# Optimization experiments

Hardware: AMD Instinct MI355X
Metric: run time of the kernel (lower is better)

Reference implementation:

```python
import jax, jax.numpy as jnp
import numpy as np

N_NODES = 50000
F_IN = 256
HEADS = 8
C = 256 // HEADS  # out channels per head (output_dim // heads)
NEG_SLOPE = 0.2


def setup_inputs() -> dict:
    key = jax.random.key(0)
    k_x, k_e, k_w, k_as, k_ad, k_b = jax.random.split(key, 6)
    x = jax.random.normal(k_x, (N_NODES, F_IN), dtype=jnp.float32)
    edge_index = jax.random.randint(k_e, (2, 800000), 0, N_NODES, dtype=jnp.int32)
    # GATConv params: linear weight, per-head attention vectors, bias
    s = 1.0 / np.sqrt(F_IN)
    W = jax.random.uniform(k_w, (F_IN, HEADS * C), jnp.float32, -s, s)
    att_src = jax.random.uniform(k_as, (HEADS, C), jnp.float32, -s, s)
    att_dst = jax.random.uniform(k_ad, (HEADS, C), jnp.float32, -s, s)
    bias = jnp.zeros((HEADS * C,), jnp.float32)
    return {"x": x, "edge_index": edge_index, "W": W,
            "att_src": att_src, "att_dst": att_dst, "bias": bias}


def _gat_forward(x, edge_index, W, att_src, att_dst, bias):
    N = x.shape[0]
    # add self loops (PyG GATConv default add_self_loops=True)
    loops = jnp.arange(N, dtype=edge_index.dtype)
    src = jnp.concatenate([edge_index[0], loops])
    dst = jnp.concatenate([edge_index[1], loops])

    h = (x @ W).reshape(N, HEADS, C)                       # [N,H,C]
    a_src = jnp.einsum('nhc,hc->nh', h, att_src)           # [N,H]
    a_dst = jnp.einsum('nhc,hc->nh', h, att_dst)           # [N,H]

    alpha = a_src[src] + a_dst[dst]                        # [E2,H]
    alpha = jax.nn.leaky_relu(alpha, NEG_SLOPE)
    # softmax over incoming edges of each dst node, per head
    amax = jax.ops.segment_max(alpha, dst, num_segments=N)
    amax = jnp.where(jnp.isfinite(amax), amax, 0.0)
    ex = jnp.exp(alpha - amax[dst])
    denom = jax.ops.segment_sum(ex, dst, num_segments=N) + 1e-16
    attn = ex / denom[dst]                                 # [E2,H]

    msg = h[src] * attn[:, :, None]                        # [E2,H,C]
    out = jax.ops.segment_sum(msg, dst, num_segments=N)    # [N,H,C]
    out = out.reshape(N, HEADS * C) + bias
    return jax.nn.elu(out)


def reference(x, edge_index, W, att_src, att_dst, bias):
    return _gat_forward(x, edge_index, W, att_src, att_dst, bias)
```

## Files before the change

kernel.cpp:

```cpp
#include <hip/hip_runtime.h>
#include <hip/hip_bf16.h>
#include <math.h>

#define F_IN 256
#define HEADS 8
#define CPH 32
#define NEG_SLOPE 0.2f
#define MAXD 128

typedef short bf16x8 __attribute__((ext_vector_type(8)));
typedef float f32x4  __attribute__((ext_vector_type(4)));
typedef _Float16 half4 __attribute__((ext_vector_type(4)));

static __device__ __forceinline__ unsigned short f2bf(float f) {
    union { float f; unsigned int u; } v; v.f = f;
    unsigned int r = (v.u + 0x7FFFu + ((v.u >> 16) & 1u)) >> 16;
    return (unsigned short)r;
}
static __device__ __forceinline__ float bf2f(unsigned short h) {
    union { unsigned int u; float f; } v; v.u = ((unsigned int)h) << 16;
    return v.f;
}

static __device__ __forceinline__ void lds_fence() {
    asm volatile("s_waitcnt lgkmcnt(0)" ::: "memory");
    __builtin_amdgcn_sched_barrier(0);
}

__global__ __launch_bounds__(256) void wprep_kernel(
    const float* __restrict__ W, short* __restrict__ WtHi, short* __restrict__ WtLo)
{
    const int k = blockIdx.x;
    const int n = threadIdx.x;
    const float w = W[(size_t)k * 256 + n];
    const unsigned short h = f2bf(w);
    const unsigned short l = f2bf(w - bf2f(h));
    const int step = k >> 5, kg = (k >> 3) & 3, j = k & 7;
    const size_t dst = ((((size_t)step * 4 + kg) * 256) + n) * 8 + j;
    WtHi[dst] = (short)h;
    WtLo[dst] = (short)l;
}

__global__ __launch_bounds__(256, 2) void gemm_mfma_kernel(
    const float* __restrict__ X, const short* __restrict__ WtHi,
    const short* __restrict__ WtLo, _Float16* __restrict__ H2, int M)
{
    __shared__ short Ah[4][128][8];
    __shared__ short Al[4][128][8];
    __shared__ short Bh[4][128][8];
    __shared__ short Bl[4][128][8];

    const int t    = threadIdx.x;
    const int lane = t & 63;
    const int wid  = t >> 6;
    const int wr   = wid >> 1;
    const int wc   = wid & 1;
    const int row0 = blockIdx.x * 128;
    const int col0 = blockIdx.y * 128;

    const int srow  = t >> 1;
    const int shalf = t & 1;

    f32x4 acc[4][4];
#pragma unroll
    for (int i = 0; i < 4; ++i)
#pragma unroll
        for (int j = 0; j < 4; ++j)
            acc[i][j] = (f32x4){0.f, 0.f, 0.f, 0.f};

    const int kgf = lane >> 4;
    const int lrow = lane & 15;

    for (int step = 0; step < 8; ++step) {
        const int k0 = step * 32;
        float f[16];
        const int grow = row0 + srow;
        if (grow < M) {
            const float4* xp = (const float4*)(X + (size_t)grow * 256 + k0 + shalf * 16);
            const float4 v0 = xp[0], v1 = xp[1], v2 = xp[2], v3 = xp[3];
            f[0] = v0.x; f[1] = v0.y; f[2]  = v0.z; f[3]  = v0.w;
            f[4] = v1.x; f[5] = v1.y; f[6]  = v1.z; f[7]  = v1.w;
            f[8] = v2.x; f[9] = v2.y; f[10] = v2.z; f[11] = v2.w;
            f[12] = v3.x; f[13] = v3.y; f[14] = v3.z; f[15] = v3.w;
        } else {
#pragma unroll
            for (int j = 0; j < 16; ++j) f[j] = 0.f;
        }
#pragma unroll
        for (int c = 0; c < 2; ++c) {
            bf16x8 hi, lo;
#pragma unroll
            for (int j = 0; j < 8; ++j) {
                const float x = f[c * 8 + j];
                const unsigned short hb = f2bf(x);
                hi[j] = (short)hb;
                lo[j] = (short)f2bf(x - bf2f(hb));
            }
            const int kg = shalf * 2 + c;
            *(bf16x8*)&Ah[kg][srow][0] = hi;
            *(bf16x8*)&Al[kg][srow][0] = lo;
        }
#pragma unroll
        for (int rep = 0; rep < 2; ++rep) {
            const int s  = t + rep * 256;
            const int kg = s >> 7;
            const int nl = s & 127;
            const size_t src = ((((size_t)step * 4 + kg) * 256) + col0 + nl) * 8;
            *(bf16x8*)&Bh[kg][nl][0] = *(const bf16x8*)&WtHi[src];
            *(bf16x8*)&Bl[kg][nl][0] = *(const bf16x8*)&WtLo[src];
        }
        __syncthreads();

        bf16x8 ah[4], al[4];
#pragma unroll
        for (int i = 0; i < 4; ++i) {
            const int rl = wr * 64 + i * 16 + lrow;
            ah[i] = *(const bf16x8*)&Ah[kgf][rl][0];
            al[i] = *(const bf16x8*)&Al[kgf][rl][0];
        }
#pragma unroll
        for (int j = 0; j < 4; ++j) {
            const int cl = wc * 64 + j * 16 + lrow;
            const bf16x8 bh = *(const bf16x8*)&Bh[kgf][cl][0];
            const bf16x8 bl = *(const bf16x8*)&Bl[kgf][cl][0];
#pragma unroll
            for (int i = 0; i < 4; ++i) {
                acc[i][j] = __builtin_amdgcn_mfma_f32_16x16x32_bf16(al[i], bh, acc[i][j], 0, 0, 0);
                acc[i][j] = __builtin_amdgcn_mfma_f32_16x16x32_bf16(ah[i], bl, acc[i][j], 0, 0, 0);
                acc[i][j] = __builtin_amdgcn_mfma_f32_16x16x32_bf16(ah[i], bh, acc[i][j], 0, 0, 0);
            }
        }
        __syncthreads();
    }

    const int cbase = col0 + wc * 64 + lrow;
    const int rbase = row0 + wr * 64 + (lane >> 4) * 4;
#pragma unroll
    for (int i = 0; i < 4; ++i) {
#pragma unroll
        for (int r = 0; r < 4; ++r) {
            const int row = rbase + i * 16 + r;
            if (row < M) {
#pragma unroll
                for (int j = 0; j < 4; ++j)
                    H2[(size_t)row * 256 + cbase + j * 16] = (_Float16)acc[i][j][r];
            }
        }
    }
}

__global__ __launch_bounds__(256) void attdot_kernel(
    const _Float16* __restrict__ H2, const float* __restrict__ att_src,
    const float* __restrict__ att_dst, float* __restrict__ a_src,
    float* __restrict__ a_dst, int N)
{
    const int n = (int)((blockIdx.x * blockDim.x + threadIdx.x) >> 6);
    const int lane = threadIdx.x & 63;
    if (n >= N) return;
    const half4 hv = *(const half4*)(H2 + (size_t)n * 256 + lane * 4);
    const float4 as = *(const float4*)(att_src + lane * 4);
    const float4 ad = *(const float4*)(att_dst + lane * 4);
    const float h0 = (float)hv[0], h1 = (float)hv[1], h2 = (float)hv[2], h3 = (float)hv[3];
    float s = h0 * as.x + h1 * as.y + h2 * as.z + h3 * as.w;
    float d = h0 * ad.x + h1 * ad.y + h2 * ad.z + h3 * ad.w;
#pragma unroll
    for (int off = 1; off < 8; off <<= 1) {
        s += __shfl_xor(s, off);
        d += __shfl_xor(d, off);
    }
    if ((lane & 7) == 0) {
        a_src[(size_t)n * 8 + (lane >> 3)] = s;
        a_dst[(size_t)n * 8 + (lane >> 3)] = d;
    }
}

__global__ __launch_bounds__(256) void hist_kernel(
    const int* __restrict__ ei, int* __restrict__ deg, int E, int E2)
{
    const int e = blockIdx.x * blockDim.x + threadIdx.x;
    if (e >= E2) return;
    const int dst = (e < E) ? ei[(size_t)E + e] : (e - E);
    atomicAdd(&deg[dst], 1);
}

__global__ __launch_bounds__(256) void scan_reduce_kernel(
    const int* __restrict__ deg, int* __restrict__ partial, int n)
{
    const int i = blockIdx.x * 256 + threadIdx.x;
    int v = (i < n) ? deg[i] : 0;
#pragma unroll
    for (int off = 1; off < 64; off <<= 1) v += __shfl_xor(v, off);
    __shared__ int s[4];
    if ((threadIdx.x & 63) == 0) s[threadIdx.x >> 6] = v;
    __syncthreads();
    if (threadIdx.x == 0) partial[blockIdx.x] = s[0] + s[1] + s[2] + s[3];
}

__global__ __launch_bounds__(256) void scan_partials_kernel(
    int* __restrict__ partial, int nb)
{
    __shared__ int tmp[256];
    const int t = threadIdx.x;
    const int v = (t < nb) ? partial[t] : 0;
    tmp[t] = v;
    __syncthreads();
    for (int off = 1; off < 256; off <<= 1) {
        int add = (t >= off) ? tmp[t - off] : 0;
        __syncthreads();
        tmp[t] += add;
        __syncthreads();
    }
    if (t < nb) partial[t] = tmp[t] - v;
}

__global__ __launch_bounds__(256) void scan_final_kernel(
    const int* __restrict__ deg, const int* __restrict__ partial,
    int* __restrict__ offsets, int n, int total)
{
    __shared__ int tmp[256];
    const int t = threadIdx.x;
    const int i = blockIdx.x * 256 + t;
    const int v = (i < n) ? deg[i] : 0;
    tmp[t] = v;
    __syncthreads();
    for (int off = 1; off < 256; off <<= 1) {
        int add = (t >= off) ? tmp[t - off] : 0;
        __syncthreads();
        tmp[t] += add;
        __syncthreads();
    }
    if (i < n) offsets[i] = partial[blockIdx.x] + tmp[t] - v;
    if (i == 0) offsets[n] = total;
}

__global__ __launch_bounds__(256) void scatter_kernel(
    const int* __restrict__ ei, const int* __restrict__ offsets,
    int* __restrict__ cursor, int* __restrict__ sorted_src, int E, int E2)
{
    const int e = blockIdx.x * blockDim.x + threadIdx.x;
    if (e >= E2) return;
    int src, dst;
    if (e < E) { src = ei[e]; dst = ei[(size_t)E + e]; }
    else       { src = e - E; dst = e - E; }
    const int pos = atomicAdd(&cursor[dst], 1);
    sorted_src[offsets[dst] + pos] = src;
}

__global__ __launch_bounds__(256) void aggregate_kernel(
    const _Float16* __restrict__ H2, const float* __restrict__ Asrc,
    const float* __restrict__ Adst, const int* __restrict__ offsets,
    const int* __restrict__ sorted_src, const float* __restrict__ bias,
    float* __restrict__ out, int N)
{
    __shared__ float aw[4][MAXD][8];
    __shared__ int   sid[4][MAXD];

    const int n = (int)((blockIdx.x * blockDim.x + threadIdx.x) >> 6);
    const int lane = threadIdx.x & 63;
    const int wid  = (threadIdx.x >> 6) & 3;
    if (n >= N) return;

    const int beg = offsets[n];
    const int deg = offsets[n + 1] - beg;
    const int dcap = deg < MAXD ? deg : MAXD;

    const int h2 = lane & 7;
    const float adst2 = Adst[(size_t)n * 8 + h2];

    float m = -INFINITY;
    for (int i = lane; i < deg * 8; i += 64) {
        const int e = i >> 3;
        const int s = sorted_src[beg + e];
        float a = Asrc[(size_t)s * 8 + h2] + adst2;
        a = a > 0.f ? a : NEG_SLOPE * a;
        if (e < MAXD) {
            aw[wid][e][h2] = a;
            if (h2 == 0) sid[wid][e] = s;
        }
        m = fmaxf(m, a);
    }
#pragma unroll
    for (int off = 8; off < 64; off <<= 1) m = fmaxf(m, __shfl_xor(m, off));
    lds_fence();

    float ssum = 0.f;
    for (int i = lane; i < deg * 8; i += 64) {
        const int e = i >> 3;
        float a;
        if (e < MAXD) {
            a = aw[wid][e][h2];
        } else {
            const int s = sorted_src[beg + e];
            a = Asrc[(size_t)s * 8 + h2] + adst2;
            a = a > 0.f ? a : NEG_SLOPE * a;
        }
        const float w = __expf(a - m);
        ssum += w;
        if (e < MAXD) aw[wid][e][h2] = w;
    }
#pragma unroll
    for (int off = 8; off < 64; off <<= 1) ssum += __shfl_xor(ssum, off);
    const float rdn = 1.f / (ssum + 1e-16f);
    lds_fence();

    for (int i = lane; i < dcap * 8; i += 64)
        aw[wid][i >> 3][h2] *= rdn;
    lds_fence();

    const int h3 = lane >> 3;
    const float m3   = __shfl(m, h3);
    const float rdn3 = __shfl(rdn, h3);
    const float adst3 = __shfl(adst2, h3);

    float4 acc0 = make_float4(0.f, 0.f, 0.f, 0.f);
    float4 acc1 = make_float4(0.f, 0.f, 0.f, 0.f);
    int e = 0;
    for (; e + 4 <= dcap; e += 4) {
        const int4 s4 = *(const int4*)&sid[wid][e];
        const float w0 = aw[wid][e + 0][h3];
        const float w1 = aw[wid][e + 1][h3];
        const float w2 = aw[wid][e + 2][h3];
        const float w3 = aw[wid][e + 3][h3];
        const half4 g0 = *(const half4*)(H2 + (size_t)s4.x * 256 + lane * 4);
        const half4 g1 = *(const half4*)(H2 + (size_t)s4.y * 256 + lane * 4);
        const half4 g2 = *(const half4*)(H2 + (size_t)s4.z * 256 + lane * 4);
        const half4 g3 = *(const half4*)(H2 + (size_t)s4.w * 256 + lane * 4);
        acc0.x += (float)g0[0] * w0; acc0.y += (float)g0[1] * w0; acc0.z += (float)g0[2] * w0; acc0.w += (float)g0[3] * w0;
        acc1.x += (float)g1[0] * w1; acc1.y += (float)g1[1] * w1; acc1.z += (float)g1[2] * w1; acc1.w += (float)g1[3] * w1;
        acc0.x += (float)g2[0] * w2; acc0.y += (float)g2[1] * w2; acc0.z += (float)g2[2] * w2; acc0.w += (float)g2[3] * w2;
        acc1.x += (float)g3[0] * w3; acc1.y += (float)g3[1] * w3; acc1.z += (float)g3[2] * w3; acc1.w += (float)g3[3] * w3;
    }
    for (; e < dcap; ++e) {
        const int s0 = sid[wid][e];
        const float w0 = aw[wid][e][h3];
        const half4 g0 = *(const half4*)(H2 + (size_t)s0 * 256 + lane * 4);
        acc0.x += (float)g0[0] * w0; acc0.y += (float)g0[1] * w0; acc0.z += (float)g0[2] * w0; acc0.w += (float)g0[3] * w0;
    }
    for (; e < deg; ++e) {
        const int s0 = sorted_src[beg + e];
        float a0 = Asrc[(size_t)s0 * 8 + h3] + adst3;
        a0 = a0 > 0.f ? a0 : NEG_SLOPE * a0;
        const float w0 = __expf(a0 - m3) * rdn3;
        const half4 g0 = *(const half4*)(H2 + (size_t)s0 * 256 + lane * 4);
        acc0.x += (float)g0[0] * w0; acc0.y += (float)g0[1] * w0; acc0.z += (float)g0[2] * w0; acc0.w += (float)g0[3] * w0;
    }
    float4 acc;
    acc.x = acc0.x + acc1.x; acc.y = acc0.y + acc1.y;
    acc.z = acc0.z + acc1.z; acc.w = acc0.w + acc1.w;

    const float4 b = *(const float4*)(bias + lane * 4);
    float4 o;
    o.x = acc.x + b.x; o.y = acc.y + b.y; o.z = acc.z + b.z; o.w = acc.w + b.w;
    o.x = o.x > 0.f ? o.x : __expf(o.x) - 1.f;
    o.y = o.y > 0.f ? o.y : __expf(o.y) - 1.f;
    o.z = o.z > 0.f ? o.z : __expf(o.z) - 1.f;
    o.w = o.w > 0.f ? o.w : __expf(o.w) - 1.f;
    *(float4*)(out + (size_t)n * 256 + lane * 4) = o;
}

extern "C" void kernel_launch(void* const* d_in, const int* in_sizes, int n_in,
                              void* d_out, int out_size, void* d_ws, size_t ws_size,
                              hipStream_t stream)
{
    const float* x       = (const float*)d_in[0];
    const int*   ei      = (const int*)  d_in[1];
    const float* W       = (const float*)d_in[2];
    const float* att_src = (const float*)d_in[3];
    const float* att_dst = (const float*)d_in[4];
    const float* bias    = (const float*)d_in[5];
    float* out = (float*)d_out;

    const int N  = in_sizes[0] / F_IN;
    const int E  = in_sizes[1] / 2;
    const int E2 = E + N;
    const int NB = (N + 255) / 256;

    char* ws = (char*)d_ws;
    size_t o = 0;
    auto take = [&](size_t bytes) { void* p = ws + o; o = (o + bytes + 255) & ~(size_t)255; return p; };
    _Float16* H2      = (_Float16*)take((size_t)N * 256 * 2);
    float* a_src      = (float*)take((size_t)N * 8 * 4);
    float* a_dst      = (float*)take((size_t)N * 8 * 4);
    int*   deg        = (int*)  take((size_t)N * 4 * 2);
    int*   cursor     = deg + N;
    int*   offsets    = (int*)  take((size_t)(N + 1) * 4);
    int*   sorted_src = (int*)  take((size_t)E2 * 4);
    int*   partial    = (int*)  take((size_t)NB * 4);
    short* WtHi       = (short*)take((size_t)256 * 256 * 2);
    short* WtLo       = (short*)take((size_t)256 * 256 * 2);
    (void)ws_size; (void)n_in; (void)out_size;

    hipMemsetAsync(deg, 0, (size_t)N * 4 * 2, stream);

    wprep_kernel<<<256, 256, 0, stream>>>(W, WtHi, WtLo);
    dim3 ggrid((N + 127) / 128, 2);
    gemm_mfma_kernel<<<ggrid, 256, 0, stream>>>(x, WtHi, WtLo, H2, N);

    attdot_kernel<<<(N * 64 + 255) / 256, 256, 0, stream>>>(H2, att_src, att_dst, a_src, a_dst, N);

    hist_kernel<<<(E2 + 255) / 256, 256, 0, stream>>>(ei, deg, E, E2);
    scan_reduce_kernel<<<NB, 256, 0, stream>>>(deg, partial, N);
    scan_partials_kernel<<<1, 256, 0, stream>>>(partial, NB);
    scan_final_kernel<<<NB, 256, 0, stream>>>(deg, partial, offsets, N, E2);
    scatter_kernel<<<(E2 + 255) / 256, 256, 0, stream>>>(ei, offsets, cursor, sorted_src, E, E2);

    aggregate_kernel<<<(N * 64 + 255) / 256, 256, 0, stream>>>(H2, a_src, a_dst, offsets, sorted_src, bias, out, N);
}
```

Measured before the change: 300.3 us.

## Switch GEMM to single-pass fp16 MFMA, fuse prep/hist, single-pass decoupled scan

The split-bf16 three-MFMA GEMM becomes a single fp16 MFMA pass over a 512-thread block that covers all 256 output columns, so X is read and converted only once. Weight conversion and the degree histogram are merged into one launch. The three-kernel prefix scan becomes a single decoupled-lookback scan that uses a ticket counter. The aggregate kernel drops its separate LDS normalization pass and applies the reciprocal denominator inline. These cut launch count and GEMM arithmetic, but fp16 rounding of X and W loses accuracy and range compared with the fp32-emulating bf16 split.

```diff
diff --git a/kernel.cpp b/kernel.cpp
--- a/kernel.cpp
+++ b/kernel.cpp
@@ -4,62 +4,52 @@
 
 #define F_IN 256
 #define HEADS 8
-#define CPH 32
 #define NEG_SLOPE 0.2f
 #define MAXD 128
 
-typedef short bf16x8 __attribute__((ext_vector_type(8)));
 typedef float f32x4  __attribute__((ext_vector_type(4)));
+typedef _Float16 f16x8 __attribute__((ext_vector_type(8)));
 typedef _Float16 half4 __attribute__((ext_vector_type(4)));
-
-static __device__ __forceinline__ unsigned short f2bf(float f) {
-    union { float f; unsigned int u; } v; v.f = f;
-    unsigned int r = (v.u + 0x7FFFu + ((v.u >> 16) & 1u)) >> 16;
-    return (unsigned short)r;
-}
-static __device__ __forceinline__ float bf2f(unsigned short h) {
-    union { unsigned int u; float f; } v; v.u = ((unsigned int)h) << 16;
-    return v.f;
-}
 
 static __device__ __forceinline__ void lds_fence() {
     asm volatile("s_waitcnt lgkmcnt(0)" ::: "memory");
     __builtin_amdgcn_sched_barrier(0);
 }
 
-__global__ __launch_bounds__(256) void wprep_kernel(
-    const float* __restrict__ W, short* __restrict__ WtHi, short* __restrict__ WtLo)
-{
-    const int k = blockIdx.x;
-    const int n = threadIdx.x;
-    const float w = W[(size_t)k * 256 + n];
-    const unsigned short h = f2bf(w);
-    const unsigned short l = f2bf(w - bf2f(h));
-    const int step = k >> 5, kg = (k >> 3) & 3, j = k & 7;
-    const size_t dst = ((((size_t)step * 4 + kg) * 256) + n) * 8 + j;
-    WtHi[dst] = (short)h;
-    WtLo[dst] = (short)l;
-}
-
-__global__ __launch_bounds__(256, 2) void gemm_mfma_kernel(
-    const float* __restrict__ X, const short* __restrict__ WtHi,
-    const short* __restrict__ WtLo, _Float16* __restrict__ H2, int M)
-{
-    __shared__ short Ah[4][128][8];
-    __shared__ short Al[4][128][8];
-    __shared__ short Bh[4][128][8];
-    __shared__ short Bl[4][128][8];
+__global__ __launch_bounds__(256) void prep_hist_kernel(
+    const float* __restrict__ W, _Float16* __restrict__ Wt,
+    const int* __restrict__ ei, int* __restrict__ deg, int E, int E2, int nhist)
+{
+    if ((int)blockIdx.x < nhist) {
+        const int e = blockIdx.x * 256 + threadIdx.x;
+        if (e >= E2) return;
+        const int dst = (e < E) ? ei[(size_t)E + e] : (e - E);
+        atomicAdd(&deg[dst], 1);
+    } else {
+        const int k = blockIdx.x - nhist;
+        const int n = threadIdx.x;
+        const float w = W[(size_t)k * 256 + n];
+        const int step = k >> 5, kg = (k >> 3) & 3, j = k & 7;
+        Wt[((((size_t)step * 4 + kg) * 256) + n) * 8 + j] = (_Float16)w;
+    }
+}
+
+__global__ __launch_bounds__(512, 4) void gemm_f16_kernel(
+    const float* __restrict__ X, const _Float16* __restrict__ Wt,
+    _Float16* __restrict__ H2, int M)
+{
+    __shared__ _Float16 Ah[4][128][8];
+    __shared__ _Float16 Bh[4][256][8];
 
     const int t    = threadIdx.x;
     const int lane = t & 63;
     const int wid  = t >> 6;
-    const int wr   = wid >> 1;
-    const int wc   = wid & 1;
+    const int wr   = wid >> 2;
+    const int wc   = wid & 3;
     const int row0 = blockIdx.x * 128;
-    const int col0 = blockIdx.y * 128;
-
-    const int srow  = t >> 1;
-    const int shalf = t & 1;
+
+    const int akg  = t >> 7;
+    const int arow = t & 127;
 
     f32x4 acc[4][4];
 #pragma unroll
@@ -68,72 +58,49 @@
         for (int j = 0; j < 4; ++j)
             acc[i][j] = (f32x4){0.f, 0.f, 0.f, 0.f};
 
-    const int kgf = lane >> 4;
+    const int kgf  = lane >> 4;
     const int lrow = lane & 15;
 
     for (int step = 0; step < 8; ++step) {
-        const int k0 = step * 32;
-        float f[16];
-        const int grow = row0 + srow;
+        const int grow = row0 + arow;
+        float4 v0 = make_float4(0.f, 0.f, 0.f, 0.f);
+        float4 v1 = make_float4(0.f, 0.f, 0.f, 0.f);
         if (grow < M) {
-            const float4* xp = (const float4*)(X + (size_t)grow * 256 + k0 + shalf * 16);
-            const float4 v0 = xp[0], v1 = xp[1], v2 = xp[2], v3 = xp[3];
-            f[0] = v0.x; f[1] = v0.y; f[2]  = v0.z; f[3]  = v0.w;
-            f[4] = v1.x; f[5] = v1.y; f[6]  = v1.z; f[7]  = v1.w;
-            f[8] = v2.x; f[9] = v2.y; f[10] = v2.z; f[11] = v2.w;
-            f[12] = v3.x; f[13] = v3.y; f[14] = v3.z; f[15] = v3.w;
-        } else {
-#pragma unroll
-            for (int j = 0; j < 16; ++j) f[j] = 0.f;
-        }
-#pragma unroll
-        for (int c = 0; c < 2; ++c) {
-            bf16x8 hi, lo;
-#pragma unroll
-            for (int j = 0; j < 8; ++j) {
-                const float x = f[c * 8 + j];
-                const unsigned short hb = f2bf(x);
-                hi[j] = (short)hb;
-                lo[j] = (short)f2bf(x - bf2f(hb));
-            }
-            const int kg = shalf * 2 + c;
-            *(bf16x8*)&Ah[kg][srow][0] = hi;
-            *(bf16x8*)&Al[kg][srow][0] = lo;
-        }
+            const float* xp = X + (size_t)grow * 256 + step * 32 + akg * 8;
+            v0 = *(const float4*)xp;
+            v1 = *(const float4*)(xp + 4);
+        }
+        f16x8 a;
+        a[0] = (_Float16)v0.x; a[1] = (_Float16)v0.y;
+        a[2] = (_Float16)v0.z; a[3] = (_Float16)v0.w;
+        a[4] = (_Float16)v1.x; a[5] = (_Float16)v1.y;
+        a[6] = (_Float16)v1.z; a[7] = (_Float16)v1.w;
+        *(f16x8*)&Ah[akg][arow][0] = a;
 #pragma unroll
         for (int rep = 0; rep < 2; ++rep) {
-            const int s  = t + rep * 256;
-            const int kg = s >> 7;
-            const int nl = s & 127;
-            const size_t src = ((((size_t)step * 4 + kg) * 256) + col0 + nl) * 8;
-            *(bf16x8*)&Bh[kg][nl][0] = *(const bf16x8*)&WtHi[src];
-            *(bf16x8*)&Bl[kg][nl][0] = *(const bf16x8*)&WtLo[src];
+            const int s  = t + rep * 512;
+            const int kg = s >> 8;
+            const int nl = s & 255;
+            *(f16x8*)&Bh[kg][nl][0] =
+                *(const f16x8*)&Wt[((((size_t)step * 4 + kg) * 256) + nl) * 8];
         }
         __syncthreads();
 
-        bf16x8 ah[4], al[4];
-#pragma unroll
-        for (int i = 0; i < 4; ++i) {
-            const int rl = wr * 64 + i * 16 + lrow;
-            ah[i] = *(const bf16x8*)&Ah[kgf][rl][0];
-            al[i] = *(const bf16x8*)&Al[kgf][rl][0];
-        }
+        f16x8 af[4];
+#pragma unroll
+        for (int i = 0; i < 4; ++i)
+            af[i] = *(const f16x8*)&Ah[kgf][wr * 64 + i * 16 + lrow][0];
 #pragma unroll
         for (int j = 0; j < 4; ++j) {
-            const int cl = wc * 64 + j * 16 + lrow;
-            const bf16x8 bh = *(const bf16x8*)&Bh[kgf][cl][0];
-            const bf16x8 bl = *(const bf16x8*)&Bl[kgf][cl][0];
-#pragma unroll
-            for (int i = 0; i < 4; ++i) {
-                acc[i][j] = __builtin_amdgcn_mfma_f32_16x16x32_bf16(al[i], bh, acc[i][j], 0, 0, 0);
-                acc[i][j] = __builtin_amdgcn_mfma_f32_16x16x32_bf16(ah[i], bl, acc[i][j], 0, 0, 0);
-                acc[i][j] = __builtin_amdgcn_mfma_f32_16x16x32_bf16(ah[i], bh, acc[i][j], 0, 0, 0);
-            }
+            const f16x8 bf = *(const f16x8*)&Bh[kgf][wc * 64 + j * 16 + lrow][0];
+#pragma unroll
+            for (int i = 0; i < 4; ++i)
+                acc[i][j] = __builtin_amdgcn_mfma_f32_16x16x32_f16(af[i], bf, acc[i][j], 0, 0, 0);
         }
         __syncthreads();
     }
 
-    const int cbase = col0 + wc * 64 + lrow;
+    const int cbase = wc * 64 + lrow;
     const int rbase = row0 + wr * 64 + (lane >> 4) * 4;
 #pragma unroll
     for (int i = 0; i < 4; ++i) {
@@ -174,62 +141,55 @@
     }
 }
 
-__global__ __launch_bounds__(256) void hist_kernel(
-    const int* __restrict__ ei, int* __restrict__ deg, int E, int E2)
-{
-    const int e = blockIdx.x * blockDim.x + threadIdx.x;
-    if (e >= E2) return;
-    const int dst = (e < E) ? ei[(size_t)E + e] : (e - E);
-    atomicAdd(&deg[dst], 1);
-}
-
-__global__ __launch_bounds__(256) void scan_reduce_kernel(
-    const int* __restrict__ deg, int* __restrict__ partial, int n)
-{
-    const int i = blockIdx.x * 256 + threadIdx.x;
-    int v = (i < n) ? deg[i] : 0;
-#pragma unroll
-    for (int off = 1; off < 64; off <<= 1) v += __shfl_xor(v, off);
-    __shared__ int s[4];
-    if ((threadIdx.x & 63) == 0) s[threadIdx.x >> 6] = v;
+__global__ __launch_bounds__(256) void scan_onepass_kernel(
+    const int* __restrict__ deg, int* __restrict__ offsets,
+    int* __restrict__ status, int* __restrict__ ticket, int n, int total)
+{
+    __shared__ int tmp[256];
+    __shared__ int s_bid;
+    __shared__ int s_prev;
+    const int t = threadIdx.x;
+    if (t == 0) s_bid = atomicAdd(ticket, 1);
     __syncthreads();
-    if (threadIdx.x == 0) partial[blockIdx.x] = s[0] + s[1] + s[2] + s[3];
-}
-
-__global__ __launch_bounds__(256) void scan_partials_kernel(
-    int* __restrict__ partial, int nb)
-{
-    __shared__ int tmp[256];
-    const int t = threadIdx.x;
-    const int v = (t < nb) ? partial[t] : 0;
+    const int bid = s_bid;
+    const int i = bid * 256 + t;
+    const int v = (i < n) ? deg[i] : 0;
     tmp[t] = v;
     __syncthreads();
+    int x = v;
     for (int off = 1; off < 256; off <<= 1) {
         int add = (t >= off) ? tmp[t - off] : 0;
         __syncthreads();
-        tmp[t] += add;
+        x += add;
+        tmp[t] = x;
         __syncthreads();
     }
-    if (t < nb) partial[t] = tmp[t] - v;
-}
-
-__global__ __launch_bounds__(256) void scan_final_kernel(
-    const int* __restrict__ deg, const int* __restrict__ partial,
-    int* __restrict__ offsets, int n, int total)
-{
-    __shared__ int tmp[256];
-    const int t = threadIdx.x;
-    const int i = blockIdx.x * 256 + t;
-    const int v = (i < n) ? deg[i] : 0;
-    tmp[t] = v;
+    const int bsum = tmp[255];
+    if (t == 0) {
+        if (bid == 0) {
+            __hip_atomic_store(&status[0], (bsum << 2) | 2,
+                               __ATOMIC_RELEASE, __HIP_MEMORY_SCOPE_AGENT);
+            s_prev = 0;
+        } else {
+            __hip_atomic_store(&status[bid], (bsum << 2) | 1,
+                               __ATOMIC_RELEASE, __HIP_MEMORY_SCOPE_AGENT);
+            int run = 0;
+            int p = bid - 1;
+            while (true) {
+                const int st = __hip_atomic_load(&status[p],
+                                   __ATOMIC_ACQUIRE, __HIP_MEMORY_SCOPE_AGENT);
+                if ((st & 3) == 0) { __builtin_amdgcn_s_sleep(1); continue; }
+                run += (st >> 2);
+                if ((st & 3) == 2) break;
+                --p;
+            }
+            __hip_atomic_store(&status[bid], ((run + bsum) << 2) | 2,
+                               __ATOMIC_RELEASE, __HIP_MEMORY_SCOPE_AGENT);
+            s_prev = run;
+        }
+    }
     __syncthreads();
-    for (int off = 1; off < 256; off <<= 1) {
-        int add = (t >= off) ? tmp[t - off] : 0;
-        __syncthreads();
-        tmp[t] += add;
-        __syncthreads();
-    }
-    if (i < n) offsets[i] = partial[blockIdx.x] + tmp[t] - v;
+    if (i < n) offsets[i] = s_prev + x - v;
     if (i == 0) offsets[n] = total;
 }
 
@@ -303,13 +263,9 @@
     const float rdn = 1.f / (ssum + 1e-16f);
     lds_fence();
 
-    for (int i = lane; i < dcap * 8; i += 64)
-        aw[wid][i >> 3][h2] *= rdn;
-    lds_fence();
-
     const int h3 = lane >> 3;
-    const float m3   = __shfl(m, h3);
-    const float rdn3 = __shfl(rdn, h3);
+    const float m3    = __shfl(m, h3);
+    const float rdn3  = __shfl(rdn, h3);
     const float adst3 = __shfl(adst2, h3);
 
     float4 acc0 = make_float4(0.f, 0.f, 0.f, 0.f);
@@ -317,10 +273,10 @@
     int e = 0;
     for (; e + 4 <= dcap; e += 4) {
         const int4 s4 = *(const int4*)&sid[wid][e];
-        const float w0 = aw[wid][e + 0][h3];
-        const float w1 = aw[wid][e + 1][h3];
-        const float w2 = aw[wid][e + 2][h3];
-        const float w3 = aw[wid][e + 3][h3];
+        const float w0 = aw[wid][e + 0][h3] * rdn3;
+        const float w1 = aw[wid][e + 1][h3] * rdn3;
+        const float w2 = aw[wid][e + 2][h3] * rdn3;
+        const float w3 = aw[wid][e + 3][h3] * rdn3;
         const half4 g0 = *(const half4*)(H2 + (size_t)s4.x * 256 + lane * 4);
         const half4 g1 = *(const half4*)(H2 + (size_t)s4.y * 256 + lane * 4);
         const half4 g2 = *(const half4*)(H2 + (size_t)s4.z * 256 + lane * 4);
@@ -332,7 +288,7 @@
     }
     for (; e < dcap; ++e) {
         const int s0 = sid[wid][e];
-        const float w0 = aw[wid][e][h3];
+        const float w0 = aw[wid][e][h3] * rdn3;
         const half4 g0 = *(const half4*)(H2 + (size_t)s0 * 256 + lane * 4);
         acc0.x += (float)g0[0] * w0; acc0.y += (float)g0[1] * w0; acc0.z += (float)g0[2] * w0; acc0.w += (float)g0[3] * w0;
     }
@@ -374,6 +330,7 @@
     const int E  = in_sizes[1] / 2;
     const int E2 = E + N;
     const int NB = (N + 255) / 256;
+    const int NHIST = (E2 + 255) / 256;
 
     char* ws = (char*)d_ws;
     size_t o = 0;
@@ -381,27 +338,25 @@
     _Float16* H2      = (_Float16*)take((size_t)N * 256 * 2);
     float* a_src      = (float*)take((size_t)N * 8 * 4);
     float* a_dst      = (float*)take((size_t)N * 8 * 4);
-    int*   deg        = (int*)  take((size_t)N * 4 * 2);
-    int*   cursor     = deg + N;
+    int*   meta       = (int*)  take((size_t)(2 * N + NB + 8) * 4);
+    int*   deg        = meta;
+    int*   cursor     = meta + N;
+    int*   status     = meta + 2 * N;
+    int*   ticket     = meta + 2 * N + NB;
     int*   offsets    = (int*)  take((size_t)(N + 1) * 4);
     int*   sorted_src = (int*)  take((size_t)E2 * 4);
-    int*   partial    = (int*)  take((size_t)NB * 4);
-    short* WtHi       = (short*)take((size_t)256 * 256 * 2);
-    short* WtLo       = (short*)take((size_t)256 * 256 * 2);
+    _Float16* Wt      = (_Float16*)take((size_t)256 * 256 * 2);
     (void)ws_size; (void)n_in; (void)out_size;
 
-    hipMemsetAsync(deg, 0, (size_t)N * 4 * 2, stream);
-
-    wprep_kernel<<<256, 256, 0, stream>>>(W, WtHi, WtLo);
-    dim3 ggrid((N + 127) / 128, 2);
-    gemm_mfma_kernel<<<ggrid, 256, 0, stream>>>(x, WtHi, WtLo, H2, N);
+    hipMemsetAsync(meta, 0, (size_t)(2 * N + NB + 8) * 4, stream);
+
+    prep_hist_kernel<<<NHIST + 256, 256, 0, stream>>>(W, Wt, ei, deg, E, E2, NHIST);
+
+    gemm_f16_kernel<<<(N + 127) / 128, 512, 0, stream>>>(x, Wt, H2, N);
 
     attdot_kernel<<<(N * 64 + 255) / 256, 256, 0, stream>>>(H2, att_src, att_dst, a_src, a_dst, N);
 
-    hist_kernel<<<(E2 + 255) / 256, 256, 0, stream>>>(ei, deg, E, E2);
-    scan_reduce_kernel<<<NB, 256, 0, stream>>>(deg, partial, N);
-    scan_partials_kernel<<<1, 256, 0, stream>>>(partial, NB);
-    scan_final_kernel<<<NB, 256, 0, stream>>>(deg, partial, offsets, N, E2);
+    scan_onepass_kernel<<<NB, 256, 0, stream>>>(deg, offsets, status, ticket, N, E2);
     scatter_kernel<<<(E2 + 255) / 256, 256, 0, stream>>>(ei, offsets, cursor, sorted_src, E, E2);
 
     aggregate_kernel<<<(N * 64 + 255) / 256, 256, 0, stream>>>(H2, a_src, a_dst, offsets, sorted_src, bias, out, N);
```

Measured after the change: 315.6 us. 5.1% more time.
